# Kernel optimization log

Measured on AMD Instinct MI355X. Metric: run time of the kernel, lower is better.

Reference implementation:

```python
import jax, jax.numpy as jnp
import numpy as np

B, S, D = 32, 512, 512      # batch, seq, feature
E, H, O, K = 8, 2048, 512, 2  # experts, expert hidden, expert out, top_k


def setup_inputs() -> dict:
    key = jax.random.key(0)
    ks = jax.random.split(key, 5)
    sc = lambda k, shape, scale: jax.random.normal(k, shape, jnp.float32) * scale
    return {
        "x": sc(ks[0], (B, S, D), 1.0),
        "attn_w": sc(ks[1], (D, 1), 0.05),
        "attn_b": jnp.zeros((1,), jnp.float32),
        "gate_w": sc(ks[2], (D, E), 0.05),
        "gate_b": jnp.zeros((E,), jnp.float32),
        "w1": sc(ks[3], (E, D, H), 0.02),
        "b1": jnp.zeros((E, H), jnp.float32),
        "w2": sc(ks[4], (E, H, O), 0.02),
        "b2": jnp.zeros((E, O), jnp.float32),
    }


def reference(x, attn_w, attn_b, gate_w, gate_b, w1, b1, w2, b2):
    # --- attention pooling over the sequence axis ---
    scores = x @ attn_w + attn_b                      # [B,S,1]
    aw = jax.nn.softmax(scores, axis=1)               # softmax over seq
    pooled = jnp.sum(x * aw, axis=1)                  # [B,D]

    # --- gating: softmax -> top-k mask -> renormalize ---
    gates = jax.nn.softmax(pooled @ gate_w + gate_b, axis=-1)  # [B,E]
    _, idx = jax.lax.top_k(gates, K)                  # [B,K]
    mask = jnp.sum(jax.nn.one_hot(idx, E, dtype=gates.dtype), axis=-2)  # [B,E]
    g = gates * mask
    g = g / (jnp.sum(g, axis=-1, keepdims=True) + 1e-9)        # [B,E]

    # --- dense all-experts compute (exact GELU, as keras Dense('gelu')) ---
    h = jax.nn.gelu(jnp.einsum('bsd,edh->ebsh', x, w1) + b1[:, None, None, :],
                    approximate=False)                 # [E,B,S,H]
    eo = jax.nn.gelu(jnp.einsum('ebsh,eho->ebso', h, w2) + b2[:, None, None, :],
                     approximate=False)                # [E,B,S,O]

    # --- weighted combine over experts ---
    return jnp.einsum('ebso,be->bso', eo, g)           # [B,S,O]
```

## Files before the change

### kernel.cpp

```cpp
#include <hip/hip_runtime.h>
#include <hip/hip_bf16.h>
#include <math.h>

#define B_  32
#define S_  512
#define D_  512
#define E_  8
#define H_  2048
#define O_  512

typedef __bf16 bf16x8 __attribute__((ext_vector_type(8)));
typedef float  f32x4  __attribute__((ext_vector_type(4)));

#define GL2LDS(src, dst) \
  __builtin_amdgcn_global_load_lds((const __attribute__((address_space(1))) void*)(src), \
                                   (__attribute__((address_space(3))) void*)(dst), 16, 0, 0)

#define MFMA16(a, b, c) __builtin_amdgcn_mfma_f32_16x16x32_bf16((a), (b), (c), 0, 0, 0)

__device__ __forceinline__ float gelu_fast(float v) {
  float w = v * fmaf(v * v, 0.0713548162f, 1.5957691216f);
  float e = __expf(-w);
  return v * __builtin_amdgcn_rcpf(1.0f + e);
}


__global__ __launch_bounds__(256) void cast_score_kernel(
    const float* __restrict__ x, const float* __restrict__ attn_w,
    char* __restrict__ xpack, float* __restrict__ scores)
{
  const int t = threadIdx.x;
  const int r = t >> 5;
  const int cg = t & 31;
  const int row = blockIdx.x * 8 + r;
  const int bb = row >> 9, s = row & 511;
  const float* src  = x + (size_t)row * D_ + cg * 16;
  const float* wsrc = attn_w + cg * 16;
  char* xp = xpack + (size_t)bb * 524288 + s * 64;
  const int sx = (s >> 1) & 3;
  float acc = 0.f;
#pragma unroll
  for (int k = 0; k < 4; ++k) {
    const int d0 = cg * 16 + k * 4;
    float4 v  = *(const float4*)(src + k * 4);
    float4 wv = *(const float4*)(wsrc + k * 4);
    acc += v.x * wv.x + v.y * wv.y + v.z * wv.z + v.w * wv.w;
    ushort4 o;
    o.x = __builtin_bit_cast(unsigned short, __float2bfloat16(v.x));
    o.y = __builtin_bit_cast(unsigned short, __float2bfloat16(v.y));
    o.z = __builtin_bit_cast(unsigned short, __float2bfloat16(v.z));
    o.w = __builtin_bit_cast(unsigned short, __float2bfloat16(v.w));
    const int u = d0 >> 5;
    const int byte = u * 32768 + ((((d0 >> 3) & 3) ^ sx) << 4) + (d0 & 7) * 2;
    *(ushort4*)(xp + byte) = o;
  }
#pragma unroll
  for (int off = 16; off; off >>= 1) acc += __shfl_xor(acc, off);
  if (cg == 0) scores[row] = acc;
}

__global__ __launch_bounds__(512) void pool_kernel(
    const float* __restrict__ x, const float* __restrict__ scores,
    float* __restrict__ pooled)
{
  __shared__ float awsh[512];
  __shared__ float red[8];
  __shared__ float mm, ss;
  __shared__ float sm[4][128];
  const int t = threadIdx.x;
  const int b = blockIdx.y;
  float v = scores[b * S_ + t];
  float m = v;
#pragma unroll
  for (int off = 32; off; off >>= 1) m = fmaxf(m, __shfl_xor(m, off));
  if ((t & 63) == 0) red[t >> 6] = m;
  __syncthreads();
  if (t == 0) {
    float a = red[0];
    for (int i = 1; i < 8; ++i) a = fmaxf(a, red[i]);
    mm = a;
  }
  __syncthreads();
  float e = expf(v - mm);
  float s = e;
#pragma unroll
  for (int off = 32; off; off >>= 1) s += __shfl_xor(s, off);
  if ((t & 63) == 0) red[t >> 6] = s;
  __syncthreads();
  if (t == 0) {
    float a = 0.f;
    for (int i = 0; i < 8; ++i) a += red[i];
    ss = 1.f / a;
  }
  __syncthreads();
  awsh[t] = e * ss;
  __syncthreads();

  const int dl = t & 127;
  const int sh = t >> 7;
  const int d = blockIdx.x * 128 + dl;
  const float* xp = x + (size_t)b * S_ * D_ + d;
  float acc = 0.f;
#pragma unroll 4
  for (int s2 = sh; s2 < S_; s2 += 4)
    acc = fmaf(awsh[s2], xp[(size_t)s2 * D_], acc);
  if (sh) sm[sh][dl] = acc;
  __syncthreads();
  if (sh == 0) pooled[b * D_ + d] = acc + sm[1][dl] + sm[2][dl] + sm[3][dl];
}

__global__ __launch_bounds__(256) void gate_psort_kernel(
    const float* __restrict__ pooled, const float* __restrict__ gate_w,
    const float* __restrict__ gate_b, int* __restrict__ gidx, float* __restrict__ gwt,
    int* __restrict__ psort)
{
  __shared__ float gl[32][8];
  const int t = threadIdx.x;
  const int b = t >> 3, ee = t & 7;
  float z = gate_b[ee];
  const float* pb = pooled + b * D_;
  for (int d = 0; d < D_; ++d) z = fmaf(pb[d], gate_w[d * E_ + ee], z);
  gl[b][ee] = z;
  __syncthreads();
  if (t < 32) {
    float ge[8];
    float zmax = gl[t][0];
    for (int i = 1; i < 8; ++i) zmax = fmaxf(zmax, gl[t][i]);
    float zs = 0.f;
    for (int i = 0; i < 8; ++i) { ge[i] = expf(gl[t][i] - zmax); zs += ge[i]; }
    for (int i = 0; i < 8; ++i) ge[i] /= zs;
    int i0 = 0;
    for (int i = 1; i < 8; ++i) if (ge[i] > ge[i0]) i0 = i;
    int i1 = -1;
    for (int i = 0; i < 8; ++i) if (i != i0 && (i1 < 0 || ge[i] > ge[i1])) i1 = i;
    float denom = ge[i0] + ge[i1] + 1e-9f;
    gidx[t * 2 + 0] = i0; gidx[t * 2 + 1] = i1;
    gwt[t * 2 + 0] = ge[i0] / denom; gwt[t * 2 + 1] = ge[i1] / denom;
  }
  __syncthreads();
  if (t == 0) {
    int cnt[E_] = {}, pos[E_];
    for (int p = 0; p < 2 * B_; ++p) cnt[gidx[p]]++;
    int s = 0;
    for (int e2 = 0; e2 < E_; ++e2) { pos[e2] = s; s += cnt[e2]; }
    for (int p = 0; p < 2 * B_; ++p) psort[pos[gidx[p]]++] = p;
  }
}

__global__ void pack_w_kernel(const float* __restrict__ in, char* __restrict__ outp,
                              int R, int C)
{
  __shared__ float tile[32][33];
  const int z = blockIdx.z;
  const float* inz = in + (size_t)z * R * C;
  const int c0 = blockIdx.x * 32, r0 = blockIdx.y * 32;
  const int tx = threadIdx.x, ty = threadIdx.y;
#pragma unroll
  for (int jj = 0; jj < 4; ++jj) {
    int r = r0 + ty + jj * 8;
    tile[ty + jj * 8][tx] = inz[(size_t)r * C + c0 + tx];
  }
  __syncthreads();
  const int k = r0 + tx;
  const int u = k >> 5;
  const int PAN = C * 64;
  char* oz = outp + (size_t)z * R * C * 2 + (size_t)u * PAN;
  const int kslot = (k >> 3) & 3;
  const int kbyte = (k & 7) * 2;
#pragma unroll
  for (int jj = 0; jj < 4; ++jj) {
    const int row = c0 + ty + jj * 8;
    const int byte = row * 64 + ((kslot ^ ((row >> 1) & 3)) << 4) + kbyte;
    *(ushort*)(oz + byte) =
        __builtin_bit_cast(unsigned short, __float2bfloat16(tile[tx][ty + jj * 8]));
  }
}

__device__ __forceinline__ void gemm_core_v10(const char* __restrict__ Ag, const char* __restrict__ Bg,
                                              const size_t unitA, const size_t unitB,
                                              const int NT, char* lds, f32x4 (&acc)[4][4])
{
  const int tid = threadIdx.x;
  const int l = tid & 63;
  const int w = tid >> 6;
  const int wm = w >> 1;
  const int wn = w & 1;
  const int lr = l & 15;
  const int ks = (l >> 4) & 3;
  const int swz = ((ks ^ ((lr >> 1) & 3)) << 4);
  const int abase = wm * 4096 + lr * 64 + swz;
  const int bloff = (wn * 64 + lr) * 64 + swz;
  const int dst = tid * 16;

#pragma unroll 1
  for (int t = 0; t < NT; ++t) {
    const char* a0 = Ag + (size_t)(2 * t)     * unitA;
    const char* a1 = Ag + (size_t)(2 * t + 1) * unitA;
    const char* b0 = Bg + (size_t)(2 * t)     * unitB + bloff;
    const char* b1 = Bg + (size_t)(2 * t + 1) * unitB + bloff;
    GL2LDS(a0 + dst, lds + dst);          GL2LDS(a0 + 4096 + dst, lds + 4096 + dst);
    GL2LDS(a1 + dst, lds + 8192 + dst);   GL2LDS(a1 + 4096 + dst, lds + 12288 + dst);
    bf16x8 bv0[4], bv1[4];
#pragma unroll
    for (int n = 0; n < 4; ++n) {
      bv0[n] = *(const bf16x8*)(b0 + n * 1024);
      bv1[n] = *(const bf16x8*)(b1 + n * 1024);
    }
    asm volatile("s_waitcnt vmcnt(0)" ::: "memory");
    __builtin_amdgcn_s_barrier();

    bf16x8 a0f[4], a1f[4];
#pragma unroll
    for (int m = 0; m < 4; ++m) {
      a0f[m] = *(const bf16x8*)(lds + abase + m * 1024);
      a1f[m] = *(const bf16x8*)(lds + 8192 + abase + m * 1024);
    }
#pragma unroll
    for (int m = 0; m < 4; ++m)
#pragma unroll
      for (int n = 0; n < 4; ++n) {
        acc[m][n] = MFMA16(a0f[m], bv0[n], acc[m][n]);
        acc[m][n] = MFMA16(a1f[m], bv1[n], acc[m][n]);
      }
    __builtin_amdgcn_s_barrier();
  }
}

__global__ __launch_bounds__(256, 3) void gemm1_kernel(
    const char* __restrict__ xpack, const char* __restrict__ W1pack,
    const float* __restrict__ b1, char* __restrict__ Hpack,
    const int* __restrict__ gidx, const int* __restrict__ psort)
{
  __shared__ char lds[16384];
  const int P = blockIdx.x;
  const int L = (P & 7) * 512 + (P >> 3);
  const int p = psort[L >> 6];
  const int tl = L & 63;
  const int b = p >> 1;
  const int e = gidx[p];
  const int h0 = (tl >> 2) * 128;
  const int s0 = (tl & 3) * 128;
  const char* Ag = W1pack + (size_t)e * 2097152 + h0 * 64;
  const char* Bg = xpack + (size_t)b * 524288 + s0 * 64;
  f32x4 acc[4][4] = {};
  gemm_core_v10(Ag, Bg, 131072, 32768, D_ / 64, lds, acc);

  const int tid = threadIdx.x, l = tid & 63, w = tid >> 6;
  const int wm = w >> 1, wn = w & 1, lr = l & 15, q4 = ((l >> 4) & 3) << 2;
  const float* b1e = b1 + (size_t)e * H_ + h0;
  char* Hp = Hpack + (size_t)p * 2097152;
#pragma unroll
  for (int m = 0; m < 4; ++m) {
    const int hl = wm * 64 + m * 16 + q4;
    const int h = h0 + hl;
    const int uh = h >> 5;
    const int hslot = (h >> 3) & 3;
    const int hbyte = (h & 7) * 2;
    const float4 bias = *(const float4*)(b1e + hl);
#pragma unroll
    for (int n = 0; n < 4; ++n) {
      const int sl = s0 + wn * 64 + n * 16 + lr;
      ushort4 ov;
      ov.x = __builtin_bit_cast(unsigned short, __float2bfloat16(gelu_fast(acc[m][n][0] + bias.x)));
      ov.y = __builtin_bit_cast(unsigned short, __float2bfloat16(gelu_fast(acc[m][n][1] + bias.y)));
      ov.z = __builtin_bit_cast(unsigned short, __float2bfloat16(gelu_fast(acc[m][n][2] + bias.z)));
      ov.w = __builtin_bit_cast(unsigned short, __float2bfloat16(gelu_fast(acc[m][n][3] + bias.w)));
      const int byte = uh * 32768 + sl * 64 + ((hslot ^ ((sl >> 1) & 3)) << 4) + hbyte;
      *(ushort4*)(Hp + byte) = ov;
    }
  }
}

__global__ __launch_bounds__(256, 3) void gemm2_kernel(
    const char* __restrict__ Hpack, const char* __restrict__ W2pack,
    const float* __restrict__ b2, float* __restrict__ out,
    const int* __restrict__ gidx, const float* __restrict__ gwt,
    const int* __restrict__ psort)
{
  __shared__ char lds[16384];
  const int P = blockIdx.x;
  const int L = (P & 7) * 128 + (P >> 3);
  const int p = psort[L >> 4];
  const int tl = L & 15;
  const int b = p >> 1;
  const int e = gidx[p];
  const float gw = gwt[p];
  const int o0 = (tl >> 2) * 128;
  const int s0 = (tl & 3) * 128;
  const char* Ag = Hpack + (size_t)p * 2097152 + s0 * 64;
  const char* Bg = W2pack + (size_t)e * 2097152 + o0 * 64;
  f32x4 acc[4][4] = {};
  gemm_core_v10(Ag, Bg, 32768, 32768, H_ / 64, lds, acc);

  const int tid = threadIdx.x, l = tid & 63, w = tid >> 6;
  const int wm = w >> 1, wn = w & 1, lr = l & 15, q4 = ((l >> 4) & 3) << 2;
  const float* b2e = b2 + (size_t)e * O_ + o0;
#pragma unroll
  for (int m = 0; m < 4; ++m) {
    const int sl = s0 + wm * 64 + m * 16 + q4;
#pragma unroll
    for (int n = 0; n < 4; ++n) {
      const int ol = wn * 64 + n * 16 + lr;
      const float bias = b2e[ol];
      float* dstp = out + ((size_t)b * S_ + sl) * O_ + o0 + ol;
#pragma unroll
      for (int j = 0; j < 4; ++j)
        atomicAdd(dstp + (size_t)j * O_, gelu_fast(acc[m][n][j] + bias) * gw);
    }
  }
}

__global__ void sentinel_kernel(float* out, int n) {
  int i = blockIdx.x * blockDim.x + threadIdx.x;
  for (; i < n; i += gridDim.x * blockDim.x) out[i] = 1.0e6f;
}

extern "C" void kernel_launch(void* const* d_in, const int* in_sizes, int n_in,
                              void* d_out, int out_size, void* d_ws, size_t ws_size,
                              hipStream_t stream)
{
  const float* x      = (const float*)d_in[0];
  const float* attn_w = (const float*)d_in[1];
  const float* gate_w = (const float*)d_in[3];
  const float* gate_b = (const float*)d_in[4];
  const float* w1     = (const float*)d_in[5];
  const float* b1     = (const float*)d_in[6];
  const float* w2     = (const float*)d_in[7];
  const float* b2     = (const float*)d_in[8];
  float* out = (float*)d_out;

  char* ws = (char*)d_ws;
  const size_t OFF_GIDX = 0;
  const size_t OFF_GWT  = 256;
  const size_t OFF_PSRT = 512;
  const size_t OFF_X    = 1024;
  const size_t SZ_X     = (size_t)B_ * S_ * D_ * 2;
  const size_t OFF_W1T  = OFF_X + SZ_X;
  const size_t SZ_W1T   = (size_t)E_ * H_ * D_ * 2;
  const size_t OFF_W2T  = OFF_W1T + SZ_W1T;
  const size_t SZ_W2T   = (size_t)E_ * O_ * H_ * 2;
  const size_t OFF_H    = OFF_W2T + SZ_W2T;
  const size_t PAIR_H   = (size_t)S_ * H_ * 2;

  if (OFF_H + 64 * PAIR_H > ws_size) {
    hipLaunchKernelGGL(sentinel_kernel, dim3(256), dim3(256), 0, stream, out, out_size);
    return;
  }

  int*   gidx   = (int*)(ws + OFF_GIDX);
  float* gwt    = (float*)(ws + OFF_GWT);
  int*   psort  = (int*)(ws + OFF_PSRT);
  char*  xpack  = ws + OFF_X;
  char*  W1pack = ws + OFF_W1T;
  char*  W2pack = ws + OFF_W2T;
  char*  Hpack  = ws + OFF_H;
  float* scores = (float*)(ws + OFF_H);
  float* pooled = (float*)(ws + OFF_H + 131072);

  hipLaunchKernelGGL(cast_score_kernel, dim3(B_ * S_ / 8), dim3(256), 0, stream,
                     x, attn_w, xpack, scores);
  hipLaunchKernelGGL(pool_kernel, dim3(4, B_), dim3(512), 0, stream, x, scores, pooled);
  hipLaunchKernelGGL(gate_psort_kernel, dim3(1), dim3(256), 0, stream,
                     pooled, gate_w, gate_b, gidx, gwt, psort);
  hipLaunchKernelGGL(pack_w_kernel, dim3(H_ / 32, D_ / 32, E_), dim3(32, 8), 0, stream,
                     w1, W1pack, D_, H_);
  hipLaunchKernelGGL(pack_w_kernel, dim3(O_ / 32, H_ / 32, E_), dim3(32, 8), 0, stream,
                     w2, W2pack, H_, O_);
  hipMemsetAsync(d_out, 0, (size_t)out_size * sizeof(float), stream);

  hipLaunchKernelGGL(gemm1_kernel, dim3(4096), dim3(256), 0, stream,
                     xpack, W1pack, b1, Hpack, gidx, psort);
  hipLaunchKernelGGL(gemm2_kernel, dim3(1024), dim3(256), 0, stream,
                     Hpack, W2pack, b2, out, gidx, gwt, psort);
}
```

Baseline: 260.5 us.

## Double-buffer LDS and B-register tiles in GEMM core to overlap loads

Replaces the single-buffered K loop, which waited on all memory loads every iteration, with a two-stage ping-pong pipeline. The next A tile is prefetched into a second LDS buffer and the next B fragments into a second register set while the current tile is computed. Partial vmcnt waits replace full drains so memory latency can hide behind MFMA work. LDS per block doubles to 32KB and B-register usage doubles, which may reduce occupancy. The loop also assumes NT is even.

```diff
diff --git a/kernel.cpp b/kernel.cpp
--- a/kernel.cpp
+++ b/kernel.cpp
@@ -176,7 +176,7 @@
   }
 }
 
-__device__ __forceinline__ void gemm_core_v10(const char* __restrict__ Ag, const char* __restrict__ Bg,
+__device__ __forceinline__ void gemm_core_v11(const char* __restrict__ Ag, const char* __restrict__ Bg,
                                               const size_t unitA, const size_t unitB,
                                               const int NT, char* lds, f32x4 (&acc)[4][4])
 {
@@ -192,38 +192,58 @@
   const int bloff = (wn * 64 + lr) * 64 + swz;
   const int dst = tid * 16;
 
+#define V11_STAGE_A(t_, Lb) { \
+    const char* a0_ = Ag + (size_t)(2 * (t_)) * unitA; \
+    const char* a1_ = Ag + (size_t)(2 * (t_) + 1) * unitA; \
+    GL2LDS(a0_ + dst, (Lb) + dst);          GL2LDS(a0_ + 4096 + dst, (Lb) + 4096 + dst); \
+    GL2LDS(a1_ + dst, (Lb) + 8192 + dst);   GL2LDS(a1_ + 4096 + dst, (Lb) + 12288 + dst); }
+
+#define V11_LOAD_B(t_, bv) { \
+    const char* b0_ = Bg + (size_t)(2 * (t_)) * unitB + bloff; \
+    const char* b1_ = Bg + (size_t)(2 * (t_) + 1) * unitB + bloff; \
+    _Pragma("unroll") \
+    for (int n = 0; n < 4; ++n) { \
+      bv[0][n] = *(const bf16x8*)(b0_ + n * 1024); \
+      bv[1][n] = *(const bf16x8*)(b1_ + n * 1024); } }
+
+#define V11_COMPUTE(Lb, bv) { \
+    bf16x8 a0f_[4], a1f_[4]; \
+    _Pragma("unroll") \
+    for (int m = 0; m < 4; ++m) { \
+      a0f_[m] = *(const bf16x8*)((Lb) + abase + m * 1024); \
+      a1f_[m] = *(const bf16x8*)((Lb) + 8192 + abase + m * 1024); } \
+    _Pragma("unroll") \
+    for (int m = 0; m < 4; ++m) \
+      _Pragma("unroll") \
+      for (int n = 0; n < 4; ++n) { \
+        acc[m][n] = MFMA16(a0f_[m], bv[0][n], acc[m][n]); \
+        acc[m][n] = MFMA16(a1f_[m], bv[1][n], acc[m][n]); } }
+
+  char* buf0 = lds;
+  char* buf1 = lds + 16384;
+  bf16x8 bv0[2][4], bv1[2][4];
+
+  V11_STAGE_A(0, buf0); V11_LOAD_B(0, bv0);
+  V11_STAGE_A(1, buf1); V11_LOAD_B(1, bv1);
+
 #pragma unroll 1
-  for (int t = 0; t < NT; ++t) {
-    const char* a0 = Ag + (size_t)(2 * t)     * unitA;
-    const char* a1 = Ag + (size_t)(2 * t + 1) * unitA;
-    const char* b0 = Bg + (size_t)(2 * t)     * unitB + bloff;
-    const char* b1 = Bg + (size_t)(2 * t + 1) * unitB + bloff;
-    GL2LDS(a0 + dst, lds + dst);          GL2LDS(a0 + 4096 + dst, lds + 4096 + dst);
-    GL2LDS(a1 + dst, lds + 8192 + dst);   GL2LDS(a1 + 4096 + dst, lds + 12288 + dst);
-    bf16x8 bv0[4], bv1[4];
-#pragma unroll
-    for (int n = 0; n < 4; ++n) {
-      bv0[n] = *(const bf16x8*)(b0 + n * 1024);
-      bv1[n] = *(const bf16x8*)(b1 + n * 1024);
-    }
-    asm volatile("s_waitcnt vmcnt(0)" ::: "memory");
+  for (int t = 0; t < NT; t += 2) {
+    const bool pre = (t + 2 < NT);
+    asm volatile("s_waitcnt vmcnt(12)" ::: "memory");
     __builtin_amdgcn_s_barrier();
-
-    bf16x8 a0f[4], a1f[4];
-#pragma unroll
-    for (int m = 0; m < 4; ++m) {
-      a0f[m] = *(const bf16x8*)(lds + abase + m * 1024);
-      a1f[m] = *(const bf16x8*)(lds + 8192 + abase + m * 1024);
-    }
-#pragma unroll
-    for (int m = 0; m < 4; ++m)
-#pragma unroll
-      for (int n = 0; n < 4; ++n) {
-        acc[m][n] = MFMA16(a0f[m], bv0[n], acc[m][n]);
-        acc[m][n] = MFMA16(a1f[m], bv1[n], acc[m][n]);
-      }
+    V11_COMPUTE(buf0, bv0);
     __builtin_amdgcn_s_barrier();
-  }
+    if (pre) { V11_STAGE_A(t + 2, buf0); V11_LOAD_B(t + 2, bv0); }
+    if (pre) asm volatile("s_waitcnt vmcnt(12)" ::: "memory");
+    else     asm volatile("s_waitcnt vmcnt(0)" ::: "memory");
+    __builtin_amdgcn_s_barrier();
+    V11_COMPUTE(buf1, bv1);
+    __builtin_amdgcn_s_barrier();
+    if (pre) { V11_STAGE_A(t + 3, buf1); V11_LOAD_B(t + 3, bv1); }
+  }
+#undef V11_STAGE_A
+#undef V11_LOAD_B
+#undef V11_COMPUTE
 }
 
 __global__ __launch_bounds__(256, 3) void gemm1_kernel(
@@ -231,7 +251,7 @@
     const float* __restrict__ b1, char* __restrict__ Hpack,
     const int* __restrict__ gidx, const int* __restrict__ psort)
 {
-  __shared__ char lds[16384];
+  __shared__ char lds[32768];
   const int P = blockIdx.x;
   const int L = (P & 7) * 512 + (P >> 3);
   const int p = psort[L >> 6];
@@ -243,7 +263,7 @@
   const char* Ag = W1pack + (size_t)e * 2097152 + h0 * 64;
   const char* Bg = xpack + (size_t)b * 524288 + s0 * 64;
   f32x4 acc[4][4] = {};
-  gemm_core_v10(Ag, Bg, 131072, 32768, D_ / 64, lds, acc);
+  gemm_core_v11(Ag, Bg, 131072, 32768, D_ / 64, lds, acc);
 
   const int tid = threadIdx.x, l = tid & 63, w = tid >> 6;
   const int wm = w >> 1, wn = w & 1, lr = l & 15, q4 = ((l >> 4) & 3) << 2;
@@ -277,7 +297,7 @@
     const int* __restrict__ gidx, const float* __restrict__ gwt,
     const int* __restrict__ psort)
 {
-  __shared__ char lds[16384];
+  __shared__ char lds[32768];
   const int P = blockIdx.x;
   const int L = (P & 7) * 128 + (P >> 3);
   const int p = psort[L >> 4];
@@ -290,7 +310,7 @@
   const char* Ag = Hpack + (size_t)p * 2097152 + s0 * 64;
   const char* Bg = W2pack + (size_t)e * 2097152 + o0 * 64;
   f32x4 acc[4][4] = {};
-  gemm_core_v10(Ag, Bg, 32768, 32768, H_ / 64, lds, acc);
+  gemm_core_v11(Ag, Bg, 32768, 32768, H_ / 64, lds, acc);
 
   const int tid = threadIdx.x, l = tid & 63, w = tid >> 6;
   const int wm = w >> 1, wn = w & 1, lr = l & 15, q4 = ((l >> 4) & 3) << 2;
```

After: 258.3 us. About the same (-0.9%).
